# Optimization experiments

Hardware: AMD Instinct MI355X
Metric: run time of the kernel (lower is better)

## Reference

```python
import jax, jax.numpy as jnp
import numpy as np

# Mamba2 defaults (mamba_ssm): d_state=64, d_conv=4, expand=2, headdim=64, ngroups=1
D_MODEL = 512
D_STATE = 64
D_CONV = 4
EXPAND = 2
HEADDIM = 64
D_INNER = EXPAND * D_MODEL            # 1024
NHEADS = D_INNER // HEADDIM           # 16
CONV_DIM = D_INNER + 2 * D_STATE      # 1152
D_IN_PROJ = 2 * D_INNER + 2 * D_STATE + NHEADS  # 2192
BATCH, SEQLEN, CHUNK = 4, 4096, 64


def setup_inputs() -> dict:
    key = jax.random.key(0)
    ks = jax.random.split(key, 8)
    return {
        "x": jax.random.normal(ks[0], (BATCH, SEQLEN, D_MODEL), jnp.float32),
        "ln_w": jnp.ones((D_MODEL,), jnp.float32),
        "ln_b": jnp.zeros((D_MODEL,), jnp.float32),
        "in_w": jax.random.normal(ks[1], (D_MODEL, D_IN_PROJ), jnp.float32) * (D_MODEL ** -0.5),
        "conv_w": jax.random.normal(ks[2], (CONV_DIM, D_CONV), jnp.float32) * (D_CONV ** -0.5),
        "conv_b": jnp.zeros((CONV_DIM,), jnp.float32),
        "dt_bias": jnp.log(jnp.expm1(jax.random.uniform(ks[3], (NHEADS,), jnp.float32, 0.001, 0.1))),
        "A_log": jnp.log(jax.random.uniform(ks[4], (NHEADS,), jnp.float32, 1.0, 16.0)),
        "D": jnp.ones((NHEADS,), jnp.float32),
        "rms_w": jnp.ones((D_INNER,), jnp.float32),
        "out_w": jax.random.normal(ks[5], (D_INNER, D_MODEL), jnp.float32) * (D_INNER ** -0.5),
    }


def _layernorm(x, w, b, eps=1e-5):
    mu = jnp.mean(x, axis=-1, keepdims=True)
    var = jnp.mean((x - mu) ** 2, axis=-1, keepdims=True)
    return (x - mu) * jax.lax.rsqrt(var + eps) * w + b


def _causal_dwconv(x, w, b):  # x [B,L,C], w [C,K], b [C]
    K = w.shape[1]
    xp = jnp.pad(x, ((0, 0), (K - 1, 0), (0, 0)))
    L = x.shape[1]
    out = sum(xp[:, k:k + L, :] * w[None, None, :, k] for k in range(K))
    return out + b


def _ssd(xh, dt, Bm, Cm, A):
    # Chunked SSD (Mamba2 algorithm). xh [B,L,H,P], dt [B,L,H], Bm/Cm [B,L,N], A [H] (negative)
    b, l, h, p = xh.shape
    nc, cs = l // CHUNK, CHUNK
    Xd = (xh * dt[..., None]).reshape(b, nc, cs, h, p)
    Bc = Bm.reshape(b, nc, cs, -1)
    Cc = Cm.reshape(b, nc, cs, -1)
    Ac = (dt * A).reshape(b, nc, cs, h).transpose(0, 3, 1, 2)  # [B,H,nC,cs]
    Acum = jnp.cumsum(Ac, axis=-1)                              # [B,H,nC,cs]
    # intra-chunk (diagonal blocks)
    mask = jnp.tril(jnp.ones((cs, cs), bool))
    seg = Acum[..., :, None] - Acum[..., None, :]               # [B,H,nC,cs,cs]
    Lmat = jnp.where(mask, jnp.exp(jnp.where(mask, seg, 0.0)), 0.0)
    Y_diag = jnp.einsum('bcln,bcsn,bhcls,bcshp->bclhp', Cc, Bc, Lmat, Xd)
    # per-chunk end states
    decay = jnp.exp(Acum[..., -1:] - Acum)                      # [B,H,nC,cs]
    states = jnp.einsum('bcln,bhcl,bclhp->bchpn', Bc, decay, Xd)  # [B,nC,H,P,N]
    chunk_decay = jnp.exp(Acum[..., -1])                        # [B,H,nC]
    def step(s, inp):
        st_c, dec_c = inp
        prev = s
        s = s * dec_c[..., None, None] + st_c
        return s, prev
    _, prev = jax.lax.scan(
        step,
        jnp.zeros((b, h, p, Bc.shape[-1]), xh.dtype),
        (states.transpose(1, 0, 2, 3, 4), chunk_decay.transpose(2, 0, 1)),
    )
    prev = prev.transpose(1, 0, 2, 3, 4)                        # [B,nC,H,P,N]
    Y_off = jnp.einsum('bcln,bchpn,bhcl->bclhp', Cc, prev, jnp.exp(Acum))
    return (Y_diag + Y_off).reshape(b, l, h, p)


def reference(x, ln_w, ln_b, in_w, conv_w, conv_b, dt_bias, A_log, D, rms_w, out_w):
    b, l, _ = x.shape
    h = _layernorm(x, ln_w, ln_b)
    zxbcdt = h @ in_w                                           # [B,L,D_IN_PROJ]
    z = zxbcdt[..., :D_INNER]
    xBC = zxbcdt[..., D_INNER:D_INNER + CONV_DIM]
    dt = jax.nn.softplus(zxbcdt[..., -NHEADS:] + dt_bias)       # [B,L,H]
    xBC = jax.nn.silu(_causal_dwconv(xBC, conv_w, conv_b))
    xs = xBC[..., :D_INNER]
    Bm = xBC[..., D_INNER:D_INNER + D_STATE]
    Cm = xBC[..., D_INNER + D_STATE:]
    xh = xs.reshape(b, l, NHEADS, HEADDIM)
    A = -jnp.exp(A_log)                                         # [H]
    y = _ssd(xh, dt, Bm, Cm, A) + xh * D[None, None, :, None]
    y = y.reshape(b, l, D_INNER)
    # gated RMSNorm: rmsnorm(y * silu(z)) * rms_w
    g = y * jax.nn.silu(z)
    g = g * jax.lax.rsqrt(jnp.mean(g * g, axis=-1, keepdims=True) + 1e-5) * rms_w
    out = g @ out_w
    # dropout in eval mode = identity, drop_path=0 = identity
    return x + out
```

## Files before the change

### kernel.cpp

```cpp
#include <hip/hip_runtime.h>
#include <hip/hip_bf16.h>
#include <cstddef>

#define BATCH  4
#define SEQL   4096
#define DM     512
#define DIP    2192
#define NIP    2176
#define DI     1024
#define DST    64
#define NH     16
#define HD     64
#define CONVD  1152
#define NROWS  (BATCH*SEQL)

typedef __attribute__((ext_vector_type(8))) short short8;
typedef __attribute__((ext_vector_type(4))) float f32x4;
typedef __attribute__((ext_vector_type(4))) unsigned short u16x4;

__device__ __forceinline__ float silu_f(float v){ return v/(1.f+__expf(-v)); }

__device__ __forceinline__ unsigned short bf16_rne(float x){
  unsigned u = __float_as_uint(x);
  unsigned r = u + 0x7FFFu + ((u>>16)&1u);
  return (unsigned short)(r>>16);
}
__device__ __forceinline__ float bf16_to_f(unsigned short h){
  return __uint_as_float(((unsigned)h)<<16);
}

__global__ __launch_bounds__(256)
void k_stats(const float* __restrict__ x, const float* __restrict__ lnw,
             const float* __restrict__ lnb, float* __restrict__ stats,
             unsigned short* __restrict__ Ai){
  __shared__ float sm[8];
  int row = blockIdx.x, t = threadIdx.x;
  const float* xr = x + (size_t)row*DM;
  float v0 = xr[t], v1 = xr[t+256];
  float s = v0+v1, s2 = v0*v0+v1*v1;
  for(int o=32;o;o>>=1){ s += __shfl_down(s,o); s2 += __shfl_down(s2,o); }
  if((t&63)==0){ sm[t>>6]=s; sm[4+(t>>6)]=s2; }
  __syncthreads();
  float su = sm[0]+sm[1]+sm[2]+sm[3];
  float sq = sm[4]+sm[5]+sm[6]+sm[7];
  float mu = su*(1.f/DM);
  float rs = rsqrtf(sq*(1.f/DM) - mu*mu + 1e-5f);
  if(t==0){ stats[row*2]=mu; stats[row*2+1]=rs; }
  unsigned short* ap = Ai + (size_t)row*2*DM;
  float a0 = (v0-mu)*rs*lnw[t] + lnb[t];
  unsigned short h0 = bf16_rne(a0);
  ap[t] = h0; ap[DM+t] = bf16_rne(a0 - bf16_to_f(h0));
  float a1 = (v1-mu)*rs*lnw[t+256] + lnb[t+256];
  unsigned short h1 = bf16_rne(a1);
  ap[t+256] = h1; ap[DM+t+256] = bf16_rne(a1 - bf16_to_f(h1));
}

__global__ void k_wsplit(const float* __restrict__ src, unsigned short* __restrict__ dh,
                         unsigned short* __restrict__ dl, int K, int N, int srcStride){
  __shared__ float sm[32][33];
  int tx = threadIdx.x, ty = threadIdx.y;
  int n0 = blockIdx.x*32, k0 = blockIdx.y*32;
  #pragma unroll
  for(int j=0;j<4;j++){
    int k = k0+ty+j*8, n = n0+tx;
    sm[ty+j*8][tx] = (k<K && n<N) ? src[(size_t)k*srcStride+n] : 0.f;
  }
  __syncthreads();
  #pragma unroll
  for(int j=0;j<4;j++){
    int n = n0+ty+j*8, k = k0+tx;
    if(n < N){
      float v = sm[tx][ty+j*8];
      unsigned short hh = bf16_rne(v);
      dh[(size_t)n*K+k] = hh;
      dl[(size_t)n*K+k] = bf16_rne(v - bf16_to_f(hh));
    }
  }
}

__global__ __launch_bounds__(256)
void k_gemm_in(const unsigned short* __restrict__ Ai,
               const unsigned short* __restrict__ Bhg, const unsigned short* __restrict__ Blg,
               float* __restrict__ z, float* __restrict__ xbc){
  __shared__ unsigned short Ah[128][76], Al[128][76], Bh[128][76], Bl[128][76];
  const int ntn = NIP/128;
  int nwg = gridDim.x;
  int bid0 = blockIdx.x;
  int bid = (bid0 & 7)*(nwg>>3) + (bid0>>3);
  int tm = bid / ntn, tn = bid % ntn;
  int t = threadIdx.x, lane = t&63, wave = t>>6;
  int wr = (wave>>1)*64, wc = (wave&1)*64, fr = lane&15;
  f32x4 zero = {0.f,0.f,0.f,0.f};
  f32x4 acc[4][4];
  #pragma unroll
  for(int m=0;m<4;m++)
    #pragma unroll
    for(int n=0;n<4;n++) acc[m][n]=zero;
  const int arow = tm*128, bcol = tn*128;
  int plane = (t>>3)&1;
  unsigned short* Adst = plane ? &Al[0][0] : &Ah[0][0];
  for(int k0=0; k0<DM; k0+=64){
    __syncthreads();
    #pragma unroll
    for(int i=0;i<8;i++){
      int r = (t>>4) + i*16, c8 = (t&7)*8;
      *(short8*)(Adst + r*76 + c8) =
        *(const short8*)(Ai + ((size_t)(arow+r)*2 + plane)*DM + k0 + c8);
    }
    #pragma unroll
    for(int i=0;i<4;i++){
      int idx = t + i*256;
      int r = idx>>3, c8 = (idx&7)*8;
      *(short8*)(&Bh[r][c8]) = *(const short8*)(Bhg + (size_t)(bcol+r)*DM + k0 + c8);
      *(short8*)(&Bl[r][c8]) = *(const short8*)(Blg + (size_t)(bcol+r)*DM + k0 + c8);
    }
    __syncthreads();
    #pragma unroll
    for(int kk=0;kk<2;kk++){
      int fk = kk*32 + ((lane>>4)<<3);
      short8 afh[4], afl[4], bfh[4], bfl[4];
      #pragma unroll
      for(int m=0;m<4;m++){
        afh[m] = *(const short8*)(&Ah[wr+m*16+fr][fk]);
        afl[m] = *(const short8*)(&Al[wr+m*16+fr][fk]);
      }
      #pragma unroll
      for(int n=0;n<4;n++){
        bfh[n] = *(const short8*)(&Bh[wc+n*16+fr][fk]);
        bfl[n] = *(const short8*)(&Bl[wc+n*16+fr][fk]);
      }
      #pragma unroll
      for(int m=0;m<4;m++)
        #pragma unroll
        for(int n=0;n<4;n++){
          acc[m][n] = __builtin_amdgcn_mfma_f32_16x16x32_bf16(afh[m], bfh[n], acc[m][n], 0,0,0);
          acc[m][n] = __builtin_amdgcn_mfma_f32_16x16x32_bf16(afh[m], bfl[n], acc[m][n], 0,0,0);
          acc[m][n] = __builtin_amdgcn_mfma_f32_16x16x32_bf16(afl[m], bfh[n], acc[m][n], 0,0,0);
        }
    }
  }
  int fq = (lane>>4)*4;
  #pragma unroll
  for(int m=0;m<4;m++)
    #pragma unroll
    for(int n=0;n<4;n++)
      #pragma unroll
      for(int j=0;j<4;j++){
        int row = arow + wr + m*16 + fq + j;
        int col = bcol + wc + n*16 + fr;
        float v = acc[m][n][j];
        if(col < DI) z[(size_t)row*DI + col] = v;
        else xbc[(size_t)row*CONVD + (col-DI)] = v;
      }
}

__global__ __launch_bounds__(256)
void k_gemm_out(const unsigned short* __restrict__ gh, const unsigned short* __restrict__ gl,
                const unsigned short* __restrict__ Bhg, const unsigned short* __restrict__ Blg,
                const float* __restrict__ resid, float* __restrict__ outp){
  __shared__ unsigned short Ah[128][76], Al[128][76], Bh[128][76], Bl[128][76];
  const int ntn = DM/128;
  int nwg = gridDim.x;
  int bid0 = blockIdx.x;
  int bid = (bid0 & 7)*(nwg>>3) + (bid0>>3);
  int tm = bid / ntn, tn = bid % ntn;
  int t = threadIdx.x, lane = t&63, wave = t>>6;
  int wr = (wave>>1)*64, wc = (wave&1)*64, fr = lane&15;
  f32x4 zero = {0.f,0.f,0.f,0.f};
  f32x4 acc[4][4];
  #pragma unroll
  for(int m=0;m<4;m++)
    #pragma unroll
    for(int n=0;n<4;n++) acc[m][n]=zero;
  const int arow = tm*128, bcol = tn*128;
  int plane = (t>>3)&1;
  unsigned short* Adst = plane ? &Al[0][0] : &Ah[0][0];
  const unsigned short* gsrc = plane ? gl : gh;
  for(int k0=0; k0<DI; k0+=64){
    __syncthreads();
    #pragma unroll
    for(int i=0;i<8;i++){
      int r = (t>>4) + i*16, c8 = (t&7)*8;
      *(short8*)(Adst + r*76 + c8) =
        *(const short8*)(gsrc + (size_t)(arow+r)*DI + k0 + c8);
    }
    #pragma unroll
    for(int i=0;i<4;i++){
      int idx = t + i*256;
      int r = idx>>3, c8 = (idx&7)*8;
      *(short8*)(&Bh[r][c8]) = *(const short8*)(Bhg + (size_t)(bcol+r)*DI + k0 + c8);
      *(short8*)(&Bl[r][c8]) = *(const short8*)(Blg + (size_t)(bcol+r)*DI + k0 + c8);
    }
    __syncthreads();
    #pragma unroll
    for(int kk=0;kk<2;kk++){
      int fk = kk*32 + ((lane>>4)<<3);
      short8 afh[4], afl[4], bfh[4], bfl[4];
      #pragma unroll
      for(int m=0;m<4;m++){
        afh[m] = *(const short8*)(&Ah[wr+m*16+fr][fk]);
        afl[m] = *(const short8*)(&Al[wr+m*16+fr][fk]);
      }
      #pragma unroll
      for(int n=0;n<4;n++){
        bfh[n] = *(const short8*)(&Bh[wc+n*16+fr][fk]);
        bfl[n] = *(const short8*)(&Bl[wc+n*16+fr][fk]);
      }
      #pragma unroll
      for(int m=0;m<4;m++)
        #pragma unroll
        for(int n=0;n<4;n++){
          acc[m][n] = __builtin_amdgcn_mfma_f32_16x16x32_bf16(afh[m], bfh[n], acc[m][n], 0,0,0);
          acc[m][n] = __builtin_amdgcn_mfma_f32_16x16x32_bf16(afh[m], bfl[n], acc[m][n], 0,0,0);
          acc[m][n] = __builtin_amdgcn_mfma_f32_16x16x32_bf16(afl[m], bfh[n], acc[m][n], 0,0,0);
        }
    }
  }
  int fq = (lane>>4)*4;
  #pragma unroll
  for(int m=0;m<4;m++)
    #pragma unroll
    for(int n=0;n<4;n++)
      #pragma unroll
      for(int j=0;j<4;j++){
        int row = arow + wr + m*16 + fq + j;
        int col = bcol + wc + n*16 + fr;
        outp[(size_t)row*DM + col] = acc[m][n][j] + resid[(size_t)row*DM + col];
      }
}

__global__ __launch_bounds__(256)
void k_dt(const float* __restrict__ x, const float* __restrict__ stats,
          const float* __restrict__ lnw, const float* __restrict__ lnb,
          const float* __restrict__ in_w, const float* __restrict__ dt_bias,
          float* __restrict__ dtp){
  __shared__ float red[64];
  int row = blockIdx.x, t = threadIdx.x;
  float mu = stats[row*2], rs = stats[row*2+1];
  float a[16];
  #pragma unroll
  for(int j=0;j<16;j++) a[j]=0.f;
  #pragma unroll
  for(int i=0;i<2;i++){
    int k = t + i*256;
    float hv = (x[(size_t)row*DM + k]-mu)*rs*lnw[k] + lnb[k];
    const float* wr2 = in_w + (size_t)k*DIP + (DIP-NH);
    #pragma unroll
    for(int j=0;j<16;j++) a[j] += hv * wr2[j];
  }
  for(int o=32;o;o>>=1){
    #pragma unroll
    for(int j=0;j<16;j++) a[j] += __shfl_down(a[j],o);
  }
  if((t&63)==0){
    #pragma unroll
    for(int j=0;j<16;j++) red[(t>>6)*16+j] = a[j];
  }
  __syncthreads();
  if(t<16){
    float v = red[t] + red[16+t] + red[32+t] + red[48+t] + dt_bias[t];
    dtp[(size_t)row*NH + t] = (v > 20.f) ? v : log1pf(__expf(v));
  }
}

__global__ __launch_bounds__(256)
void k_convBC(const float* __restrict__ xbc, const float* __restrict__ cw,
              const float* __restrict__ cb, float* __restrict__ bcc){
  int gid = blockIdx.x*256 + threadIdx.x;
  int c4 = gid & 31, row = gid >> 5;
  int c = c4*4;
  int lb = row & (SEQL-1);
  const float* base = xbc + (size_t)row*CONVD + DI + c;
  f32x4 w0 = *(const f32x4*)(cw + (size_t)(DI+c+0)*4);
  f32x4 w1 = *(const f32x4*)(cw + (size_t)(DI+c+1)*4);
  f32x4 w2 = *(const f32x4*)(cw + (size_t)(DI+c+2)*4);
  f32x4 w3 = *(const f32x4*)(cw + (size_t)(DI+c+3)*4);
  f32x4 r = { cb[DI+c], cb[DI+c+1], cb[DI+c+2], cb[DI+c+3] };
  #pragma unroll
  for(int k=0;k<4;k++){
    if(lb-3+k >= 0){
      f32x4 xv = *(const f32x4*)(base + (long)(k-3)*CONVD);
      r.x += xv.x*w0[k]; r.y += xv.y*w1[k]; r.z += xv.z*w2[k]; r.w += xv.w*w3[k];
    }
  }
  r.x = silu_f(r.x); r.y = silu_f(r.y); r.z = silu_f(r.z); r.w = silu_f(r.w);
  *(f32x4*)(bcc + (size_t)row*128 + c) = r;
}

__global__ void k_acum(const float* __restrict__ dtp, const float* __restrict__ A_log,
                       float* __restrict__ acum, float* __restrict__ cdec){
  int bh = blockIdx.x;
  int h = bh & 15;
  int c = blockIdx.y, l = threadIdx.x;
  int row = (bh>>4)*SEQL + c*64 + l;
  float a = -__expf(A_log[h]);
  float v = dtp[(size_t)row*NH + h] * a;
  for(int o=1;o<64;o<<=1){ float u = __shfl_up(v,o); if(l>=o) v += u; }
  acum[(size_t)bh*SEQL + c*64 + l] = v;
  if(l==63) cdec[bh*64 + c] = __expf(v);
}

__global__ __launch_bounds__(256)
void k_states(const float* __restrict__ xbc, const float* __restrict__ bcc,
              const float* __restrict__ dtp, const float* __restrict__ acum,
              const float* __restrict__ cw, const float* __restrict__ cb,
              float* __restrict__ S){
  int h = blockIdx.x, bc = blockIdx.y;
  int b = bc >> 6, c = bc & 63;
  __shared__ float Bd[64][68];
  __shared__ float Xs[64][68];
  __shared__ float raw[67*64];
  __shared__ f32x4 wc4[64];
  __shared__ float cbv[64], acs[64], dts[64];
  int t = threadIdx.x;
  if(t < 64){
    acs[t] = acum[((size_t)(b*NH+h))*SEQL + c*64 + t];
    dts[t] = dtp[(size_t)(b*SEQL + c*64 + t)*NH + h];
    wc4[t] = *(const f32x4*)(cw + (size_t)(h*HD + t)*4);
    cbv[t] = cb[h*HD + t];
  }
  __syncthreads();
  #pragma unroll
  for(int i=0;i<4;i++){
    int idx = t + i*256;
    int l = idx>>4, n4 = (idx&15)*4;
    f32x4 bv = *(const f32x4*)(bcc + (size_t)(b*SEQL + c*64 + l)*128 + n4);
    float dec = __expf(acs[63] - acs[l]);
    *(f32x4*)&Bd[l][n4] = bv * dec;
  }
  #pragma unroll
  for(int i=0;i<5;i++){
    int idx = t + i*256;
    if(idx < 67*16){
      int rr = idx>>4, p4 = (idx&15)*4;
      int wb = c*64 - 3 + rr;
      f32x4 xv = {0.f,0.f,0.f,0.f};
      if(wb >= 0) xv = *(const f32x4*)(xbc + (size_t)(b*SEQL + wb)*CONVD + h*HD + p4);
      *(f32x4*)&raw[rr*64 + p4] = xv;
    }
  }
  __syncthreads();
  {
    int l = t>>2, q = t&3;
    float dtv = dts[l];
    #pragma unroll
    for(int jj=0;jj<16;jj++){
      int p = q*16 + jj;
      f32x4 w = wc4[p];
      float a = cbv[p] + raw[(l+0)*64+p]*w.x + raw[(l+1)*64+p]*w.y
              + raw[(l+2)*64+p]*w.z + raw[(l+3)*64+p]*w.w;
      Xs[l][p] = silu_f(a) * dtv;
    }
  }
  __syncthreads();
  int n = t>>2, p0 = (t&3)*16;
  f32x4 a0={0.f,0.f,0.f,0.f}, a1=a0, a2=a0, a3=a0;
  #pragma unroll 2
  for(int ll=0; ll<64; ll++){
    float bnd = Bd[ll][n];
    const float* xp = &Xs[ll][p0];
    a0 += bnd * *(const f32x4*)(xp);
    a1 += bnd * *(const f32x4*)(xp+4);
    a2 += bnd * *(const f32x4*)(xp+8);
    a3 += bnd * *(const f32x4*)(xp+12);
  }
  float* op = S + ((size_t)(bc*NH + h))*4096 + n*64 + p0;
  *(f32x4*)(op)    = a0;
  *(f32x4*)(op+4)  = a1;
  *(f32x4*)(op+8)  = a2;
  *(f32x4*)(op+12) = a3;
}

__global__ void k_scan(float* __restrict__ S, const float* __restrict__ cdec){
  int g = blockIdx.x*256 + threadIdx.x;
  int bh = g >> 12;
  int pn = g & 4095;
  int b = bh >> 4, h = bh & 15;
  const float* cd = cdec + bh*64;
  float s = 0.f;
  for(int c=0;c<64;c++){
    size_t idx = ((size_t)((b*64 + c)*NH + h))*4096 + pn;
    float v = S[idx];
    float d = cd[c];
    S[idx] = s;
    s = s*d + v;
  }
}

__global__ __launch_bounds__(256)
void k_y(const float* __restrict__ xbc, const float* __restrict__ bcc,
         const float* __restrict__ dtp, const float* __restrict__ acum,
         const float* __restrict__ cw, const float* __restrict__ cb,
         const float* __restrict__ Dp, float* __restrict__ Sreg){
  int h = blockIdx.x, bc = blockIdx.y;
  int b = bc >> 6, c = bc & 63;
  __shared__ float Cs[64][68];
  __shared__ float BM[64][68];
  __shared__ float Xr[64][68];
  __shared__ float PsRaw[64*68];
  __shared__ f32x4 wc4[64];
  __shared__ float cbv[64], acs[64], dts[64];
  int t = threadIdx.x;
  float* Sslot = Sreg + ((size_t)(bc*NH + h))*4096;
  if(t < 64){
    acs[t] = acum[((size_t)(b*NH+h))*SEQL + c*64 + t];
    dts[t] = dtp[(size_t)(b*SEQL + c*64 + t)*NH + h];
    wc4[t] = *(const f32x4*)(cw + (size_t)(h*HD + t)*4);
    cbv[t] = cb[h*HD + t];
  }
  #pragma unroll
  for(int i=0;i<4;i++){
    int idx = t + i*256;
    int l = idx>>4, n4 = (idx&15)*4;
    const float* bp = bcc + (size_t)(b*SEQL + c*64 + l)*128;
    *(f32x4*)&BM[l][n4] = *(const f32x4*)(bp + n4);
    *(f32x4*)&Cs[l][n4] = *(const f32x4*)(bp + 64 + n4);
  }
  #pragma unroll
  for(int i=0;i<5;i++){
    int idx = t + i*256;
    if(idx < 67*16){
      int rr = idx>>4, p4 = (idx&15)*4;
      int wb = c*64 - 3 + rr;
      f32x4 xv = {0.f,0.f,0.f,0.f};
      if(wb >= 0) xv = *(const f32x4*)(xbc + (size_t)(b*SEQL + wb)*CONVD + h*HD + p4);
      *(f32x4*)&PsRaw[rr*64 + p4] = xv;
    }
  }
  __syncthreads();
  {
    int l = t>>2, q = t&3;
    #pragma unroll
    for(int jj=0;jj<16;jj++){
      int p = q*16 + jj;
      f32x4 w = wc4[p];
      float a = cbv[p] + PsRaw[(l+0)*64+p]*w.x + PsRaw[(l+1)*64+p]*w.y
              + PsRaw[(l+2)*64+p]*w.z + PsRaw[(l+3)*64+p]*w.w;
      Xr[l][p] = silu_f(a);
    }
  }
  __syncthreads();
  int gl = t & 63, s0 = (t>>6)*16;
  float g[16];
  #pragma unroll
  for(int j=0;j<16;j++) g[j]=0.f;
  #pragma unroll 1
  for(int n4=0;n4<64;n4+=4){
    f32x4 cv = *(const f32x4*)&Cs[gl][n4];
    #pragma unroll
    for(int j=0;j<16;j++){
      f32x4 bv = *(const f32x4*)&BM[s0+j][n4];
      g[j] += cv.x*bv.x + cv.y*bv.y + cv.z*bv.z + cv.w*bv.w;
    }
  }
  __syncthreads();
  {
    float aclg = acs[gl];
    #pragma unroll
    for(int j=0;j<16;j++){
      int s = s0 + j;
      BM[gl][s] = (s <= gl) ? g[j]*__expf(aclg - acs[s])*dts[s] : 0.f;
    }
  }
  #pragma unroll
  for(int i=0;i<4;i++){
    int idx = t + i*256;
    int s = idx>>4, p4 = (idx&15)*4;
    f32x4 pv = *(const f32x4*)(Sslot + s*64 + p4);
    *(f32x4*)&PsRaw[s*68 + p4] = pv;
  }
  __syncthreads();
  {
    int l = t>>2, p0 = (t&3)*16;
    float eal = __expf(acs[l]);
    float Dh = Dp[h];
    const float* xl = &Xr[l][p0];
    f32x4 a0 = Dh * *(const f32x4*)(xl);
    f32x4 a1 = Dh * *(const f32x4*)(xl+4);
    f32x4 a2 = Dh * *(const f32x4*)(xl+8);
    f32x4 a3 = Dh * *(const f32x4*)(xl+12);
    #pragma unroll 2
    for(int s=0;s<64;s++){
      float m = BM[l][s];
      const float* xp = &Xr[s][p0];
      a0 += m * *(const f32x4*)(xp);
      a1 += m * *(const f32x4*)(xp+4);
      a2 += m * *(const f32x4*)(xp+8);
      a3 += m * *(const f32x4*)(xp+12);
    }
    #pragma unroll 2
    for(int s=0;s<64;s++){
      float cv = eal * Cs[l][s];
      const float* pp = &PsRaw[s*68 + p0];
      a0 += cv * *(const f32x4*)(pp);
      a1 += cv * *(const f32x4*)(pp+4);
      a2 += cv * *(const f32x4*)(pp+8);
      a3 += cv * *(const f32x4*)(pp+12);
    }
    float* yp = Sslot + l*64 + p0;
    *(f32x4*)(yp)    = a0;
    *(f32x4*)(yp+4)  = a1;
    *(f32x4*)(yp+8)  = a2;
    *(f32x4*)(yp+12) = a3;
  }
}

__global__ __launch_bounds__(256)
void k_gate(const float* __restrict__ Sreg, const float* __restrict__ z,
            const float* __restrict__ rms_w, unsigned short* __restrict__ gh,
            unsigned short* __restrict__ gl){
  __shared__ float sm[4];
  int row = blockIdx.x, t = threadIdx.x;
  int b = row>>12, cc = (row>>6)&63, lin = row&63;
  int h = t>>4, p = (t&15)*4;
  const float* gp = Sreg + ((size_t)((b*64+cc)*NH + h))*4096 + (size_t)lin*64 + p;
  f32x4 yv = *(const f32x4*)gp;
  f32x4 zv = *(const f32x4*)(z + (size_t)row*DI + t*4);
  f32x4 gv;
  gv.x = yv.x * silu_f(zv.x);
  gv.y = yv.y * silu_f(zv.y);
  gv.z = yv.z * silu_f(zv.z);
  gv.w = yv.w * silu_f(zv.w);
  float ss = gv.x*gv.x + gv.y*gv.y + gv.z*gv.z + gv.w*gv.w;
  for(int o=32;o;o>>=1) ss += __shfl_down(ss,o);
  if((t&63)==0) sm[t>>6] = ss;
  __syncthreads();
  float tot = sm[0]+sm[1]+sm[2]+sm[3];
  float scale = rsqrtf(tot*(1.f/DI) + 1e-5f);
  f32x4 wv = *(const f32x4*)(rms_w + t*4);
  float o0 = gv.x*scale*wv.x, o1 = gv.y*scale*wv.y;
  float o2 = gv.z*scale*wv.z, o3 = gv.w*scale*wv.w;
  u16x4 hv, lv;
  unsigned short hh;
  hh = bf16_rne(o0); hv[0]=hh; lv[0]=bf16_rne(o0-bf16_to_f(hh));
  hh = bf16_rne(o1); hv[1]=hh; lv[1]=bf16_rne(o1-bf16_to_f(hh));
  hh = bf16_rne(o2); hv[2]=hh; lv[2]=bf16_rne(o2-bf16_to_f(hh));
  hh = bf16_rne(o3); hv[3]=hh; lv[3]=bf16_rne(o3-bf16_to_f(hh));
  *(u16x4*)(gh + (size_t)row*DI + t*4) = hv;
  *(u16x4*)(gl + (size_t)row*DI + t*4) = lv;
}

extern "C" void kernel_launch(void* const* d_in, const int* in_sizes, int n_in,
                              void* d_out, int out_size, void* d_ws, size_t ws_size,
                              hipStream_t stream) {
  const float* x      = (const float*)d_in[0];
  const float* ln_w   = (const float*)d_in[1];
  const float* ln_b   = (const float*)d_in[2];
  const float* in_w   = (const float*)d_in[3];
  const float* conv_w = (const float*)d_in[4];
  const float* conv_b = (const float*)d_in[5];
  const float* dt_b   = (const float*)d_in[6];
  const float* A_log  = (const float*)d_in[7];
  const float* Dp     = (const float*)d_in[8];
  const float* rms_w  = (const float*)d_in[9];
  const float* out_w  = (const float*)d_in[10];
  float* out = (float*)d_out;
  char* ws = (char*)d_ws;

  size_t o = 0;
  float* stats = (float*)(ws+o);           o += (size_t)NROWS*2*4;
  unsigned short* w1h = (unsigned short*)(ws+o); o += (size_t)NIP*DM*2;
  unsigned short* w1l = (unsigned short*)(ws+o); o += (size_t)NIP*DM*2;
  unsigned short* w2h = (unsigned short*)(ws+o); o += (size_t)DM*DI*2;
  unsigned short* w2l = (unsigned short*)(ws+o); o += (size_t)DM*DI*2;
  float* z    = (float*)(ws+o);            o += (size_t)NROWS*DI*4;
  float* xbc  = (float*)(ws+o);            o += (size_t)NROWS*CONVD*4;
  float* dtp  = (float*)(ws+o);            o += (size_t)NROWS*NH*4;
  float* acum = (float*)(ws+o);            o += (size_t)BATCH*NH*SEQL*4;
  float* cdec = (float*)(ws+o);            o += (size_t)BATCH*NH*64*4;
  float* bcc  = (float*)(ws+o);            o += (size_t)NROWS*128*4;
  float* Sreg = (float*)(ws+o);            o += (size_t)BATCH*64*NH*4096*4;
  if(o > ws_size) return;

  unsigned short* Ai = (unsigned short*)Sreg;
  unsigned short* gh = (unsigned short*)xbc;
  unsigned short* gl = gh + (size_t)NROWS*DI;

  k_stats<<<NROWS, 256, 0, stream>>>(x, ln_w, ln_b, stats, Ai);
  k_wsplit<<<dim3(NIP/32, DM/32), dim3(32,8), 0, stream>>>(in_w,  w1h, w1l, DM, NIP, DIP);
  k_wsplit<<<dim3(DM/32,  DI/32), dim3(32,8), 0, stream>>>(out_w, w2h, w2l, DI, DM, DM);
  k_gemm_in<<<(NROWS/128)*(NIP/128), 256, 0, stream>>>(Ai, w1h, w1l, z, xbc);
  k_dt<<<NROWS, 256, 0, stream>>>(x, stats, ln_w, ln_b, in_w, dt_b, dtp);
  k_convBC<<<(NROWS*32)/256, 256, 0, stream>>>(xbc, conv_w, conv_b, bcc);
  k_acum<<<dim3(BATCH*NH, 64), 64, 0, stream>>>(dtp, A_log, acum, cdec);
  k_states<<<dim3(NH, BATCH*64), 256, 0, stream>>>(xbc, bcc, dtp, acum, conv_w, conv_b, Sreg);
  k_scan<<<(BATCH*NH*4096)/256, 256, 0, stream>>>(Sreg, cdec);
  k_y<<<dim3(NH, BATCH*64), 256, 0, stream>>>(xbc, bcc, dtp, acum, conv_w, conv_b, Dp, Sreg);
  k_gate<<<NROWS, 256, 0, stream>>>(Sreg, z, rms_w, gh, gl);
  k_gemm_out<<<(NROWS/128)*(DM/128), 256, 0, stream>>>(gh, gl, w2h, w2l, x, out);
}
```

Before: 677.9 us.

## Use split-bf16 MFMA for the intra-chunk SSD matmuls in k_y

Rewrites the per-chunk output kernel so the C·Bᵀ score matrix, the masked score times X product, and the C times previous-state product run on bf16 MFMA instructions. Operands are split into high and low bf16 parts and three MFMAs are accumulated to approximate fp32 accuracy. Shared-memory layouts change to transposed bf16 tiles, and the conv and silu step is vectorised over a reused raw buffer. This trades scalar FP32 FMA work for matrix-core throughput, at the cost of extra split and pack arithmetic, more LDS traffic, and slightly lower precision.

```diff
diff --git a/kernel.cpp b/kernel.cpp
--- a/kernel.cpp
+++ b/kernel.cpp
@@ -27,6 +27,16 @@
 }
 __device__ __forceinline__ float bf16_to_f(unsigned short h){
   return __uint_as_float(((unsigned)h)<<16);
+}
+
+__device__ __forceinline__ void split_pack4(f32x4 v, unsigned short* hp, unsigned short* lp){
+  unsigned short h0=bf16_rne(v.x), h1=bf16_rne(v.y), h2=bf16_rne(v.z), h3=bf16_rne(v.w);
+  unsigned short l0=bf16_rne(v.x-bf16_to_f(h0)), l1=bf16_rne(v.y-bf16_to_f(h1)),
+                 l2=bf16_rne(v.z-bf16_to_f(h2)), l3=bf16_rne(v.w-bf16_to_f(h3));
+  ((unsigned*)hp)[0] = (unsigned)h0 | ((unsigned)h1<<16);
+  ((unsigned*)hp)[1] = (unsigned)h2 | ((unsigned)h3<<16);
+  ((unsigned*)lp)[0] = (unsigned)l0 | ((unsigned)l1<<16);
+  ((unsigned*)lp)[1] = (unsigned)l2 | ((unsigned)l3<<16);
 }
 
 __global__ __launch_bounds__(256)
@@ -394,27 +404,37 @@
          const float* __restrict__ Dp, float* __restrict__ Sreg){
   int h = blockIdx.x, bc = blockIdx.y;
   int b = bc >> 6, c = bc & 63;
-  __shared__ float Cs[64][68];
-  __shared__ float BM[64][68];
-  __shared__ float Xr[64][68];
-  __shared__ float PsRaw[64*68];
-  __shared__ f32x4 wc4[64];
-  __shared__ float cbv[64], acs[64], dts[64];
-  int t = threadIdx.x;
+  __shared__ unsigned short Bh[64][76], Bl[64][76];
+  __shared__ unsigned short Ch[64][76], Cl[64][76];
+  __shared__ unsigned short Xth[64][76], Xtl[64][76];
+  __shared__ unsigned short Pth[64][76], Ptl[64][76];
+  __shared__ float Mbuf[64*76];
+  __shared__ float wt[4][68];
+  __shared__ float acs[64], dts[64], eals[64], cbt[64];
+  unsigned short* Mh = (unsigned short*)Mbuf;
+  unsigned short* Ml = Mh + 64*76;
+  float* raw = Mbuf;
+
+  int t = threadIdx.x, lane = t&63, wave = t>>6;
+  int fr = lane & 15, hi = lane >> 4, fq = hi*4, wr = wave*16;
   float* Sslot = Sreg + ((size_t)(bc*NH + h))*4096;
+
   if(t < 64){
-    acs[t] = acum[((size_t)(b*NH+h))*SEQL + c*64 + t];
+    float av = acum[((size_t)(b*NH+h))*SEQL + c*64 + t];
+    acs[t] = av;
+    eals[t] = __expf(av);
     dts[t] = dtp[(size_t)(b*SEQL + c*64 + t)*NH + h];
-    wc4[t] = *(const f32x4*)(cw + (size_t)(h*HD + t)*4);
-    cbv[t] = cb[h*HD + t];
+    f32x4 w = *(const f32x4*)(cw + (size_t)(h*HD + t)*4);
+    wt[0][t] = w.x; wt[1][t] = w.y; wt[2][t] = w.z; wt[3][t] = w.w;
+    cbt[t] = cb[h*HD + t];
   }
   #pragma unroll
   for(int i=0;i<4;i++){
     int idx = t + i*256;
     int l = idx>>4, n4 = (idx&15)*4;
     const float* bp = bcc + (size_t)(b*SEQL + c*64 + l)*128;
-    *(f32x4*)&BM[l][n4] = *(const f32x4*)(bp + n4);
-    *(f32x4*)&Cs[l][n4] = *(const f32x4*)(bp + 64 + n4);
+    split_pack4(*(const f32x4*)(bp + n4),      &Bh[l][n4], &Bl[l][n4]);
+    split_pack4(*(const f32x4*)(bp + 64 + n4), &Ch[l][n4], &Cl[l][n4]);
   }
   #pragma unroll
   for(int i=0;i<5;i++){
@@ -424,84 +444,112 @@
       int wb = c*64 - 3 + rr;
       f32x4 xv = {0.f,0.f,0.f,0.f};
       if(wb >= 0) xv = *(const f32x4*)(xbc + (size_t)(b*SEQL + wb)*CONVD + h*HD + p4);
-      *(f32x4*)&PsRaw[rr*64 + p4] = xv;
-    }
-  }
-  __syncthreads();
-  {
-    int l = t>>2, q = t&3;
-    #pragma unroll
-    for(int jj=0;jj<16;jj++){
-      int p = q*16 + jj;
-      f32x4 w = wc4[p];
-      float a = cbv[p] + PsRaw[(l+0)*64+p]*w.x + PsRaw[(l+1)*64+p]*w.y
-              + PsRaw[(l+2)*64+p]*w.z + PsRaw[(l+3)*64+p]*w.w;
-      Xr[l][p] = silu_f(a);
-    }
-  }
-  __syncthreads();
-  int gl = t & 63, s0 = (t>>6)*16;
-  float g[16];
-  #pragma unroll
-  for(int j=0;j<16;j++) g[j]=0.f;
-  #pragma unroll 1
-  for(int n4=0;n4<64;n4+=4){
-    f32x4 cv = *(const f32x4*)&Cs[gl][n4];
-    #pragma unroll
-    for(int j=0;j<16;j++){
-      f32x4 bv = *(const f32x4*)&BM[s0+j][n4];
-      g[j] += cv.x*bv.x + cv.y*bv.y + cv.z*bv.z + cv.w*bv.w;
-    }
-  }
-  __syncthreads();
-  {
-    float aclg = acs[gl];
-    #pragma unroll
-    for(int j=0;j<16;j++){
-      int s = s0 + j;
-      BM[gl][s] = (s <= gl) ? g[j]*__expf(aclg - acs[s])*dts[s] : 0.f;
+      *(f32x4*)&raw[rr*68 + p4] = xv;
     }
   }
   #pragma unroll
   for(int i=0;i<4;i++){
     int idx = t + i*256;
-    int s = idx>>4, p4 = (idx&15)*4;
-    f32x4 pv = *(const f32x4*)(Sslot + s*64 + p4);
-    *(f32x4*)&PsRaw[s*68 + p4] = pv;
-  }
-  __syncthreads();
+    int n = idx>>4, p4 = (idx&15)*4;
+    f32x4 pv = *(const f32x4*)(Sslot + n*64 + p4);
+    #pragma unroll
+    for(int k=0;k<4;k++){
+      float v = pv[k];
+      unsigned short hh = bf16_rne(v);
+      Pth[p4+k][n] = hh;
+      Ptl[p4+k][n] = bf16_rne(v - bf16_to_f(hh));
+    }
+  }
+  __syncthreads();
+
   {
     int l = t>>2, p0 = (t&3)*16;
-    float eal = __expf(acs[l]);
-    float Dh = Dp[h];
-    const float* xl = &Xr[l][p0];
-    f32x4 a0 = Dh * *(const f32x4*)(xl);
-    f32x4 a1 = Dh * *(const f32x4*)(xl+4);
-    f32x4 a2 = Dh * *(const f32x4*)(xl+8);
-    f32x4 a3 = Dh * *(const f32x4*)(xl+12);
-    #pragma unroll 2
-    for(int s=0;s<64;s++){
-      float m = BM[l][s];
-      const float* xp = &Xr[s][p0];
-      a0 += m * *(const f32x4*)(xp);
-      a1 += m * *(const f32x4*)(xp+4);
-      a2 += m * *(const f32x4*)(xp+8);
-      a3 += m * *(const f32x4*)(xp+12);
-    }
-    #pragma unroll 2
-    for(int s=0;s<64;s++){
-      float cv = eal * Cs[l][s];
-      const float* pp = &PsRaw[s*68 + p0];
-      a0 += cv * *(const f32x4*)(pp);
-      a1 += cv * *(const f32x4*)(pp+4);
-      a2 += cv * *(const f32x4*)(pp+8);
-      a3 += cv * *(const f32x4*)(pp+12);
-    }
-    float* yp = Sslot + l*64 + p0;
-    *(f32x4*)(yp)    = a0;
-    *(f32x4*)(yp+4)  = a1;
-    *(f32x4*)(yp+8)  = a2;
-    *(f32x4*)(yp+12) = a3;
+    f32x4 a0 = *(const f32x4*)&cbt[p0];
+    f32x4 a1 = *(const f32x4*)&cbt[p0+4];
+    f32x4 a2 = *(const f32x4*)&cbt[p0+8];
+    f32x4 a3 = *(const f32x4*)&cbt[p0+12];
+    #pragma unroll
+    for(int k=0;k<4;k++){
+      const float* rrow = &raw[(l+k)*68];
+      const float* wrow = &wt[k][0];
+      a0 += *(const f32x4*)(rrow+p0)    * *(const f32x4*)(wrow+p0);
+      a1 += *(const f32x4*)(rrow+p0+4)  * *(const f32x4*)(wrow+p0+4);
+      a2 += *(const f32x4*)(rrow+p0+8)  * *(const f32x4*)(wrow+p0+8);
+      a3 += *(const f32x4*)(rrow+p0+12) * *(const f32x4*)(wrow+p0+12);
+    }
+    f32x4 av[4] = {a0,a1,a2,a3};
+    #pragma unroll
+    for(int pe=0;pe<4;pe++)
+      #pragma unroll
+      for(int e=0;e<4;e++){
+        int p = p0 + pe*4 + e;
+        float xv = silu_f(av[pe][e]);
+        unsigned short hh = bf16_rne(xv);
+        Xth[p][l] = hh;
+        Xtl[p][l] = bf16_rne(xv - bf16_to_f(hh));
+      }
+  }
+  __syncthreads();
+
+  short8 cfh[2], cfl[2];
+  #pragma unroll
+  for(int kk=0;kk<2;kk++){
+    int fk = kk*32 + hi*8;
+    cfh[kk] = *(const short8*)&Ch[wr+fr][fk];
+    cfl[kk] = *(const short8*)&Cl[wr+fr][fk];
+  }
+  #pragma unroll 1
+  for(int sc=0; sc<4; ++sc){
+    f32x4 acc = {0.f,0.f,0.f,0.f};
+    #pragma unroll
+    for(int kk=0;kk<2;kk++){
+      int fk = kk*32 + hi*8;
+      short8 bh8 = *(const short8*)&Bh[sc*16+fr][fk];
+      short8 bl8 = *(const short8*)&Bl[sc*16+fr][fk];
+      acc = __builtin_amdgcn_mfma_f32_16x16x32_bf16(cfh[kk], bh8, acc, 0,0,0);
+      acc = __builtin_amdgcn_mfma_f32_16x16x32_bf16(cfh[kk], bl8, acc, 0,0,0);
+      acc = __builtin_amdgcn_mfma_f32_16x16x32_bf16(cfl[kk], bh8, acc, 0,0,0);
+    }
+    int s = sc*16 + fr;
+    float as_ = acs[s], ds_ = dts[s];
+    #pragma unroll
+    for(int j=0;j<4;j++){
+      int l = wr + fq + j;
+      float m = (s <= l) ? acc[j]*__expf(acs[l] - as_)*ds_ : 0.f;
+      unsigned short hh = bf16_rne(m);
+      Mh[l*76 + s] = hh;
+      Ml[l*76 + s] = bf16_rne(m - bf16_to_f(hh));
+    }
+  }
+  __syncthreads();
+
+  float Dh = Dp[h];
+  #pragma unroll 1
+  for(int pc=0; pc<4; ++pc){
+    f32x4 aD = {0.f,0.f,0.f,0.f}, aO = {0.f,0.f,0.f,0.f};
+    #pragma unroll
+    for(int kk=0;kk<2;kk++){
+      int fk = kk*32 + hi*8;
+      short8 mh8 = *(const short8*)(Mh + (wr+fr)*76 + fk);
+      short8 ml8 = *(const short8*)(Ml + (wr+fr)*76 + fk);
+      short8 xh8 = *(const short8*)&Xth[pc*16+fr][fk];
+      short8 xl8 = *(const short8*)&Xtl[pc*16+fr][fk];
+      aD = __builtin_amdgcn_mfma_f32_16x16x32_bf16(mh8, xh8, aD, 0,0,0);
+      aD = __builtin_amdgcn_mfma_f32_16x16x32_bf16(mh8, xl8, aD, 0,0,0);
+      aD = __builtin_amdgcn_mfma_f32_16x16x32_bf16(ml8, xh8, aD, 0,0,0);
+      short8 ph8 = *(const short8*)&Pth[pc*16+fr][fk];
+      short8 pl8 = *(const short8*)&Ptl[pc*16+fr][fk];
+      aO = __builtin_amdgcn_mfma_f32_16x16x32_bf16(cfh[kk], ph8, aO, 0,0,0);
+      aO = __builtin_amdgcn_mfma_f32_16x16x32_bf16(cfh[kk], pl8, aO, 0,0,0);
+      aO = __builtin_amdgcn_mfma_f32_16x16x32_bf16(cfl[kk], ph8, aO, 0,0,0);
+    }
+    int p = pc*16 + fr;
+    #pragma unroll
+    for(int j=0;j<4;j++){
+      int l = wr + fq + j;
+      float xr = bf16_to_f(Xth[p][l]) + bf16_to_f(Xtl[p][l]);
+      Sslot[l*64 + p] = aD[j] + eals[l]*aO[j] + Dh*xr;
+    }
   }
 }
 
```

New measurement: 657.6 us. -3.0%, faster.
